# Kernel tuning notes

Hardware: AMD Instinct MI355X
Metric: run time of the kernel (lower is better)

The kernel has to match this reference:

```python
import jax, jax.numpy as jnp
import numpy as np

B, L, H, E, K = 64, 200, 256, 8, 2
LN_EPS = 1e-5

def setup_inputs() -> dict:
    key = jax.random.key(0)
    ks = jax.random.split(key, 24)
    r = lambda k, *s: jax.random.normal(k, s, dtype=jnp.float32)
    w = lambda k, *s: 0.02 * jax.random.normal(k, s, dtype=jnp.float32)
    return {
        'text_emb': r(ks[0], B, L, H),
        'img_emb': r(ks[1], B, L, H),
        'item_emb': r(ks[2], B, L, H),
        'noise_t': r(ks[3], B, L, H),
        'noise_i': r(ks[4], B, L, H),
        'W_mu_t': w(ks[5], H, H), 'b_mu_t': jnp.zeros((H,), jnp.float32),
        'W_sg_t': w(ks[6], H, H), 'b_sg_t': jnp.zeros((H,), jnp.float32),
        'W_mu_i': w(ks[7], H, H), 'b_mu_i': jnp.zeros((H,), jnp.float32),
        'W_sg_i': w(ks[8], H, H), 'b_sg_i': jnp.zeros((H,), jnp.float32),
        'W_gate': w(ks[9], H, E), 'b_gate': jnp.zeros((E,), jnp.float32),
        'W_texp': w(ks[10], E, H, H), 'b_texp': jnp.zeros((E, H), jnp.float32),
        'W_iexp': w(ks[11], E, H, H), 'b_iexp': jnp.zeros((E, H), jnp.float32),
        'W_fuse': w(ks[12], 2 * H, H), 'b_fuse': jnp.zeros((H,), jnp.float32),
        'ln_g': jnp.ones((H,), jnp.float32), 'ln_b': jnp.zeros((H,), jnp.float32),
    }

def _topk_routing(z, W_gate, b_gate):
    # softmax over experts, keep top-k, renormalize (matches torch scatter_ version)
    weights = jax.nn.softmax(z @ W_gate + b_gate, axis=-1)   # [B,L,E]
    top_w, idx = jax.lax.top_k(weights, K)                   # [B,L,K]
    sparse = jnp.sum(jax.nn.one_hot(idx, E, dtype=weights.dtype) * top_w[..., None], axis=-2)
    return sparse / (jnp.sum(sparse, axis=-1, keepdims=True) + 1e-8)

def _layernorm(x, g, b):
    mu = jnp.mean(x, axis=-1, keepdims=True)
    var = jnp.mean(jnp.square(x - mu), axis=-1, keepdims=True)
    return (x - mu) * jax.lax.rsqrt(var + LN_EPS) * g + b

def reference(text_emb, img_emb, item_emb, noise_t, noise_i,
              W_mu_t, b_mu_t, W_sg_t, b_sg_t, W_mu_i, b_mu_i, W_sg_i, b_sg_i,
              W_gate, b_gate, W_texp, b_texp, W_iexp, b_iexp,
              W_fuse, b_fuse, ln_g, ln_b):
    # VAE-style reparameterization per modality
    t_mu = text_emb @ W_mu_t + b_mu_t
    t_sigma = jnp.exp(text_emb @ W_sg_t + b_sg_t)
    i_mu = img_emb @ W_mu_i + b_mu_i
    i_sigma = jnp.exp(img_emb @ W_sg_i + b_sg_i)
    t_z = t_mu + t_sigma * noise_t
    i_z = i_mu + i_sigma * noise_i
    # top-k gating
    t_gate = _topk_routing(t_z, W_gate, b_gate)   # [B,L,E]
    i_gate = _topk_routing(i_z, W_gate, b_gate)
    # dense all-expert stack + gated combine
    t_experts = jnp.einsum('blh,ehd->bled', t_z, W_texp) + b_texp  # [B,L,E,H]
    t_out = jnp.einsum('bled,ble->bld', t_experts, t_gate)
    i_experts = jnp.einsum('blh,ehd->bled', i_z, W_iexp) + b_iexp
    i_out = jnp.einsum('bled,ble->bld', i_experts, i_gate)
    # fusion: Linear(2H->H) -> LayerNorm -> ReLU, residual with item_emb
    cat = jnp.concatenate([t_out, i_out], axis=-1)
    fused = jax.nn.relu(_layernorm(cat @ W_fuse + b_fuse, ln_g, ln_b))
    fusion = item_emb + fused
    return fusion, t_mu, t_sigma, i_mu, i_sigma
```

## Files before the change

### kernel.cpp

```cpp
#include <hip/hip_runtime.h>
#include <hip/hip_bf16.h>
#include <math.h>

#define NTOK 12800
#define HD 256
#define SOUT (NTOK * HD)

typedef __attribute__((ext_vector_type(8))) short short8_t;
typedef __attribute__((ext_vector_type(4))) float f32x4;

__device__ __forceinline__ unsigned short f2b(float f) {
    union { float f; unsigned u; } v; v.f = f;
    unsigned r = (v.u + 0x7FFFu + ((v.u >> 16) & 1u)) >> 16;
    return (unsigned short)r;
}
__device__ __forceinline__ float b2f(unsigned short s) {
    union { unsigned u; float f; } v; v.u = ((unsigned)s) << 16;
    return v.f;
}
__device__ __forceinline__ void glds16(const void* g, void* l) {
    __builtin_amdgcn_global_load_lds(
        (const __attribute__((address_space(1))) void*)g,
        (__attribute__((address_space(3))) void*)l, 16, 0, 0);
}

__global__ __launch_bounds__(256) void prepW_kernel(
    const float* __restrict__ W_texp, const float* __restrict__ W_iexp,
    const float* __restrict__ W_mu_t, const float* __restrict__ W_sg_t,
    const float* __restrict__ W_mu_i, const float* __restrict__ W_sg_i,
    const float* __restrict__ W_fuse,
    unsigned short* __restrict__ wt_t, unsigned short* __restrict__ wt_i,
    unsigned short* __restrict__ wt_f,
    unsigned short* __restrict__ wpk_th, unsigned short* __restrict__ wpk_tl,
    unsigned short* __restrict__ wpk_ih, unsigned short* __restrict__ wpk_il)
{
    const int z = blockIdx.y;
    const float* src;
    unsigned short* dsth;
    unsigned short* dstl = nullptr;
    int dstride = 256, koff = 0, rowoff = 0;
    if (z < 8)       { src = W_texp + (size_t)z * 65536;       dsth = wt_t + (size_t)z * 65536; }
    else if (z < 16) { src = W_iexp + (size_t)(z - 8) * 65536; dsth = wt_i + (size_t)(z - 8) * 65536; }
    else if (z == 16){ src = W_mu_t; dsth = wpk_th; dstl = wpk_tl; }
    else if (z == 17){ src = W_sg_t; dsth = wpk_th; dstl = wpk_tl; rowoff = 256; }
    else if (z == 18){ src = W_mu_i; dsth = wpk_ih; dstl = wpk_il; }
    else if (z == 19){ src = W_sg_i; dsth = wpk_ih; dstl = wpk_il; rowoff = 256; }
    else if (z == 20){ src = W_fuse;         dsth = wt_f; dstride = 512; koff = 0;   }
    else             { src = W_fuse + 65536; dsth = wt_f; dstride = 512; koff = 256; }

    const int tk = (blockIdx.x >> 2) * 64;
    const int td = (blockIdx.x & 3) * 64;
    __shared__ float T[64][68];
    const int t = threadIdx.x;
    {
        const int r = t >> 2, c0 = (t & 3) * 16;
        const float* s = &src[(size_t)(tk + r) * 256 + td + c0];
#pragma unroll
        for (int j = 0; j < 4; ++j)
            *reinterpret_cast<float4*>(&T[r][c0 + j * 4]) =
                *reinterpret_cast<const float4*>(&s[j * 4]);
    }
    __syncthreads();
    {
        const int d = t & 63, kc = (t >> 6) * 16;
        union { unsigned short s[16]; short8_t v[2]; } uh, ul;
#pragma unroll
        for (int j = 0; j < 16; ++j) {
            const float x = T[kc + j][d];
            uh.s[j] = f2b(x);
            ul.s[j] = f2b(x - b2f(uh.s[j]));
        }
        unsigned short* p = &dsth[(size_t)(rowoff + td + d) * dstride + koff + tk + kc];
        *reinterpret_cast<short8_t*>(p) = uh.v[0];
        *reinterpret_cast<short8_t*>(p + 8) = uh.v[1];
        if (dstl) {
            unsigned short* q = &dstl[(size_t)(rowoff + td + d) * 256 + tk + kc];
            *reinterpret_cast<short8_t*>(q) = ul.v[0];
            *reinterpret_cast<short8_t*>(q + 8) = ul.v[1];
        }
    }
}

__global__ __launch_bounds__(256) void cvt_kernel(
    const float* __restrict__ text, const float* __restrict__ img,
    unsigned short* __restrict__ ah_t, unsigned short* __restrict__ al_t,
    unsigned short* __restrict__ ah_i, unsigned short* __restrict__ al_i)
{
    const int mod = blockIdx.y;
    const float* src = mod ? img : text;
    unsigned short* dh = mod ? ah_i : ah_t;
    unsigned short* dl = mod ? al_i : al_t;
    const size_t base = ((size_t)blockIdx.x * 256 + threadIdx.x) * 8;
    const float4 v0 = *reinterpret_cast<const float4*>(&src[base]);
    const float4 v1 = *reinterpret_cast<const float4*>(&src[base + 4]);
    const float x[8] = { v0.x, v0.y, v0.z, v0.w, v1.x, v1.y, v1.z, v1.w };
    union { unsigned short u[8]; short8_t v; } qh, ql;
#pragma unroll
    for (int c = 0; c < 8; ++c) {
        qh.u[c] = f2b(x[c]);
        ql.u[c] = f2b(x[c] - b2f(qh.u[c]));
    }
    *reinterpret_cast<short8_t*>(&dh[base]) = qh.v;
    *reinterpret_cast<short8_t*>(&dl[base]) = ql.v;
}

__global__ __launch_bounds__(256) void reparam_mfma_kernel(
    const unsigned short* __restrict__ ah_t, const unsigned short* __restrict__ al_t,
    const unsigned short* __restrict__ ah_i, const unsigned short* __restrict__ al_i,
    const unsigned short* __restrict__ wpk_th, const unsigned short* __restrict__ wpk_tl,
    const unsigned short* __restrict__ wpk_ih, const unsigned short* __restrict__ wpk_il,
    const float* __restrict__ b_mu_t, const float* __restrict__ b_sg_t,
    const float* __restrict__ b_mu_i, const float* __restrict__ b_sg_i,
    float* __restrict__ o_tmu, float* __restrict__ o_tsig,
    float* __restrict__ o_imu, float* __restrict__ o_isig)
{
    const int mod = blockIdx.z;
    const unsigned short* Ah = mod ? ah_i : ah_t;
    const unsigned short* Al = mod ? al_i : al_t;
    const unsigned short* Wh = mod ? wpk_ih : wpk_th;
    const unsigned short* Wl = mod ? wpk_il : wpk_tl;
    const float* bmu = mod ? b_mu_i : b_mu_t;
    const float* bsg = mod ? b_sg_i : b_sg_t;
    float* omu = mod ? o_imu : o_tmu;
    float* osg = mod ? o_isig : o_tsig;

    __shared__ __align__(16) unsigned short AhS[2][4][64][8];
    __shared__ __align__(16) unsigned short AlS[2][4][64][8];
    __shared__ __align__(16) unsigned short BhS[2][4][128][8];
    __shared__ __align__(16) unsigned short BlS[2][4][128][8];

    const int tid = threadIdx.x;
    const int lane = tid & 63;
    const int w = tid >> 6;
    const int wr = w >> 1, wc = w & 1;
    const int lg = lane >> 4;
    const int lr = lane & 15;
    const int m0 = blockIdx.x * 64;
    const int n0 = blockIdx.y * 128;

    const int ar = tid >> 2, akc = tid & 3;
    const int bn = tid >> 1, bk0 = (tid & 1) * 2;

    {
        *reinterpret_cast<short8_t*>(&AhS[0][akc][ar][0]) =
            *reinterpret_cast<const short8_t*>(&Ah[(size_t)(m0 + ar) * HD + akc * 8]);
        *reinterpret_cast<short8_t*>(&AlS[0][akc][ar][0]) =
            *reinterpret_cast<const short8_t*>(&Al[(size_t)(m0 + ar) * HD + akc * 8]);
#pragma unroll
        for (int j = 0; j < 2; ++j) {
            const int kc = bk0 + j;
            *reinterpret_cast<short8_t*>(&BhS[0][kc][bn][0]) =
                *reinterpret_cast<const short8_t*>(&Wh[(size_t)(n0 + bn) * HD + kc * 8]);
            *reinterpret_cast<short8_t*>(&BlS[0][kc][bn][0]) =
                *reinterpret_cast<const short8_t*>(&Wl[(size_t)(n0 + bn) * HD + kc * 8]);
        }
    }
    __syncthreads();

    f32x4 acc[2][4];
#pragma unroll
    for (int mi = 0; mi < 2; ++mi)
#pragma unroll
        for (int ni = 0; ni < 4; ++ni)
            acc[mi][ni] = (f32x4){0.f, 0.f, 0.f, 0.f};

    for (int ks = 0; ks < 8; ++ks) {
        const int cur = ks & 1;
        short8_t rah, ral, rbh[2], rbl[2];
        if (ks < 7) {
            const int k1 = (ks + 1) * 32;
            rah = *reinterpret_cast<const short8_t*>(&Ah[(size_t)(m0 + ar) * HD + k1 + akc * 8]);
            ral = *reinterpret_cast<const short8_t*>(&Al[(size_t)(m0 + ar) * HD + k1 + akc * 8]);
#pragma unroll
            for (int j = 0; j < 2; ++j) {
                const int kc = bk0 + j;
                rbh[j] = *reinterpret_cast<const short8_t*>(&Wh[(size_t)(n0 + bn) * HD + k1 + kc * 8]);
                rbl[j] = *reinterpret_cast<const short8_t*>(&Wl[(size_t)(n0 + bn) * HD + k1 + kc * 8]);
            }
        }
        short8_t ahf[2], alf[2], bhf[4], blf[4];
#pragma unroll
        for (int mi = 0; mi < 2; ++mi) {
            ahf[mi] = *reinterpret_cast<const short8_t*>(&AhS[cur][lg][wr * 32 + mi * 16 + lr][0]);
            alf[mi] = *reinterpret_cast<const short8_t*>(&AlS[cur][lg][wr * 32 + mi * 16 + lr][0]);
        }
#pragma unroll
        for (int ni = 0; ni < 4; ++ni) {
            bhf[ni] = *reinterpret_cast<const short8_t*>(&BhS[cur][lg][wc * 64 + ni * 16 + lr][0]);
            blf[ni] = *reinterpret_cast<const short8_t*>(&BlS[cur][lg][wc * 64 + ni * 16 + lr][0]);
        }
#pragma unroll
        for (int mi = 0; mi < 2; ++mi)
#pragma unroll
            for (int ni = 0; ni < 4; ++ni) {
                acc[mi][ni] = __builtin_amdgcn_mfma_f32_16x16x32_bf16(ahf[mi], bhf[ni], acc[mi][ni], 0, 0, 0);
                acc[mi][ni] = __builtin_amdgcn_mfma_f32_16x16x32_bf16(ahf[mi], blf[ni], acc[mi][ni], 0, 0, 0);
                acc[mi][ni] = __builtin_amdgcn_mfma_f32_16x16x32_bf16(alf[mi], bhf[ni], acc[mi][ni], 0, 0, 0);
            }
        if (ks < 7) {
            const int nxt = cur ^ 1;
            *reinterpret_cast<short8_t*>(&AhS[nxt][akc][ar][0]) = rah;
            *reinterpret_cast<short8_t*>(&AlS[nxt][akc][ar][0]) = ral;
#pragma unroll
            for (int j = 0; j < 2; ++j) {
                const int kc = bk0 + j;
                *reinterpret_cast<short8_t*>(&BhS[nxt][kc][bn][0]) = rbh[j];
                *reinterpret_cast<short8_t*>(&BlS[nxt][kc][bn][0]) = rbl[j];
            }
        }
        __syncthreads();
    }

    const bool is_sg = (n0 >= 256);
    float bv[4];
    int cc[4];
#pragma unroll
    for (int ni = 0; ni < 4; ++ni) {
        const int dpk = n0 + wc * 64 + ni * 16 + lr;
        cc[ni] = is_sg ? dpk - 256 : dpk;
        bv[ni] = is_sg ? bsg[cc[ni]] : bmu[cc[ni]];
    }
    float* outp = is_sg ? osg : omu;
#pragma unroll
    for (int mi = 0; mi < 2; ++mi)
#pragma unroll
        for (int r = 0; r < 4; ++r) {
            const int row = m0 + wr * 32 + mi * 16 + lg * 4 + r;
#pragma unroll
            for (int ni = 0; ni < 4; ++ni) {
                const float v = acc[mi][ni][r] + bv[ni];
                outp[(size_t)row * HD + cc[ni]] = is_sg ? expf(v) : v;
            }
        }
}

__global__ __launch_bounds__(256) void gate_kernel(
    const float* __restrict__ o_tmu, const float* __restrict__ o_tsig,
    const float* __restrict__ o_imu, const float* __restrict__ o_isig,
    const float* __restrict__ noise_t, const float* __restrict__ noise_i,
    const float* __restrict__ Wg, const float* __restrict__ bg,
    float* __restrict__ t_gate, float* __restrict__ i_gate,
    unsigned short* __restrict__ tzb, unsigned short* __restrict__ izb)
{
    const int mod = blockIdx.y;
    const float* mu    = mod ? o_imu  : o_tmu;
    const float* sig   = mod ? o_isig : o_tsig;
    const float* noise = mod ? noise_i : noise_t;
    float* gate        = mod ? i_gate : t_gate;
    unsigned short* zb = mod ? izb : tzb;

    const int lane = threadIdx.x & 63;
    const int n = blockIdx.x * 4 + (threadIdx.x >> 6);
    const size_t off = (size_t)n * HD + lane * 4;
    const float4 m4 = *reinterpret_cast<const float4*>(&mu[off]);
    const float4 s4 = *reinterpret_cast<const float4*>(&sig[off]);
    const float4 n4 = *reinterpret_cast<const float4*>(&noise[off]);
    const float zz[4] = { fmaf(s4.x, n4.x, m4.x), fmaf(s4.y, n4.y, m4.y),
                          fmaf(s4.z, n4.z, m4.z), fmaf(s4.w, n4.w, m4.w) };
    ushort4 zb4;
    zb4.x = f2b(zz[0]); zb4.y = f2b(zz[1]); zb4.z = f2b(zz[2]); zb4.w = f2b(zz[3]);
    *reinterpret_cast<ushort4*>(&zb[off]) = zb4;

    float lg[8];
#pragma unroll
    for (int e = 0; e < 8; ++e) lg[e] = 0.f;
#pragma unroll
    for (int i = 0; i < 4; ++i) {
        const float* wr = &Wg[(size_t)(lane * 4 + i) * 8];
        const float4 w0 = *reinterpret_cast<const float4*>(wr);
        const float4 w1 = *reinterpret_cast<const float4*>(wr + 4);
        lg[0] = fmaf(zz[i], w0.x, lg[0]); lg[1] = fmaf(zz[i], w0.y, lg[1]);
        lg[2] = fmaf(zz[i], w0.z, lg[2]); lg[3] = fmaf(zz[i], w0.w, lg[3]);
        lg[4] = fmaf(zz[i], w1.x, lg[4]); lg[5] = fmaf(zz[i], w1.y, lg[5]);
        lg[6] = fmaf(zz[i], w1.z, lg[6]); lg[7] = fmaf(zz[i], w1.w, lg[7]);
    }
#pragma unroll
    for (int off2 = 32; off2; off2 >>= 1)
#pragma unroll
        for (int e = 0; e < 8; ++e) lg[e] += __shfl_down(lg[e], off2);

    if (lane == 0) {
        float m = -1e30f;
#pragma unroll
        for (int e = 0; e < 8; ++e) { lg[e] += bg[e]; m = fmaxf(m, lg[e]); }
        float p[8], s = 0.f;
#pragma unroll
        for (int e = 0; e < 8; ++e) { p[e] = expf(lg[e] - m); s += p[e]; }
        const float inv_s = 1.f / s;
#pragma unroll
        for (int e = 0; e < 8; ++e) p[e] *= inv_s;
        int e1 = 0;
#pragma unroll
        for (int e = 1; e < 8; ++e) if (p[e] > p[e1]) e1 = e;
        int e2 = (e1 == 0) ? 1 : 0;
#pragma unroll
        for (int e = 0; e < 8; ++e) if (e != e1 && p[e] > p[e2]) e2 = e;
        const float denom = 1.f / (p[e1] + p[e2] + 1e-8f);
        float g[8];
#pragma unroll
        for (int e = 0; e < 8; ++e) g[e] = 0.f;
        g[e1] = p[e1] * denom; g[e2] = p[e2] * denom;
        float* gr = &gate[(size_t)n * 8];
        *reinterpret_cast<float4*>(gr)     = make_float4(g[0], g[1], g[2], g[3]);
        *reinterpret_cast<float4*>(gr + 4) = make_float4(g[4], g[5], g[6], g[7]);
    }
}

__global__ __launch_bounds__(256) void expert_mfma_kernel(
    const unsigned short* __restrict__ tzb, const unsigned short* __restrict__ izb,
    const unsigned short* __restrict__ wt_t, const unsigned short* __restrict__ wt_i,
    const float* __restrict__ bx_t, const float* __restrict__ bx_i,
    const float* __restrict__ g_t, const float* __restrict__ g_i,
    unsigned short* __restrict__ out_t, unsigned short* __restrict__ out_i)
{
    const int mod = blockIdx.z;
    const unsigned short* Zb = mod ? izb : tzb;
    const unsigned short* Wt = mod ? wt_i : wt_t;
    const float* bx   = mod ? bx_i : bx_t;
    const float* gate = mod ? g_i  : g_t;
    unsigned short* outp = mod ? out_i : out_t;

    __shared__ __align__(16) unsigned short Ab[2][512][8];
    __shared__ __align__(16) unsigned short Bb[2][512][8];
    __shared__ float gld[128][8];

    const int tid = threadIdx.x;
    const int lane = tid & 63;
    const int w = tid >> 6;
    const int wr = w >> 1, wc = w & 1;
    const int lg = lane >> 4;
    const int lr = lane & 15;
    const int m0 = blockIdx.x * 128;
    const int n0 = blockIdx.y * 128;

    reinterpret_cast<float4*>(&gld[0][0])[tid] =
        reinterpret_cast<const float4*>(&gate[(size_t)m0 * 8])[tid];

    const int c0 = w * 64 + lane;
    const int row0 = c0 >> 2,          kc0 = c0 & 3;
    const int row1 = (c0 + 256) >> 2,  kc1 = (c0 + 256) & 3;

#define STAGE(buf, e_, ks_)                                                    \
    {                                                                          \
        const unsigned short* We_ = Wt + (size_t)(e_) * 65536 + (size_t)n0 * HD;\
        glds16(&Zb[(size_t)(m0 + row0) * HD + (ks_) * 32 + kc0 * 8],           \
               &Ab[buf][w * 64][0]);                                           \
        glds16(&Zb[(size_t)(m0 + row1) * HD + (ks_) * 32 + kc1 * 8],           \
               &Ab[buf][256 + w * 64][0]);                                     \
        glds16(&We_[(size_t)row0 * HD + (ks_) * 32 + kc0 * 8],                 \
               &Bb[buf][w * 64][0]);                                           \
        glds16(&We_[(size_t)row1 * HD + (ks_) * 32 + kc1 * 8],                 \
               &Bb[buf][256 + w * 64][0]);                                     \
    }

    STAGE(0, 0, 0);
    __syncthreads();

    f32x4 acc[4][4], accT[4][4];
#pragma unroll
    for (int mi = 0; mi < 4; ++mi)
#pragma unroll
        for (int ni = 0; ni < 4; ++ni) {
            acc[mi][ni]  = (f32x4){0.f, 0.f, 0.f, 0.f};
            accT[mi][ni] = (f32x4){0.f, 0.f, 0.f, 0.f};
        }

    for (int kk = 0; kk < 64; ++kk) {
        const int cur = kk & 1;
        const int e = kk >> 3, ks = kk & 7;
        if (kk < 63) {
            const int e2 = (kk + 1) >> 3, ks2 = (kk + 1) & 7;
            STAGE(cur ^ 1, e2, ks2);
        }
        short8_t af[4], bf[4];
#pragma unroll
        for (int mi = 0; mi < 4; ++mi)
            af[mi] = *reinterpret_cast<const short8_t*>(
                &Ab[cur][(wr * 64 + mi * 16 + lr) * 4 + lg][0]);
#pragma unroll
        for (int ni = 0; ni < 4; ++ni)
            bf[ni] = *reinterpret_cast<const short8_t*>(
                &Bb[cur][(wc * 64 + ni * 16 + lr) * 4 + lg][0]);
#pragma unroll
        for (int mi = 0; mi < 4; ++mi)
#pragma unroll
            for (int ni = 0; ni < 4; ++ni)
                acc[mi][ni] = __builtin_amdgcn_mfma_f32_16x16x32_bf16(
                    af[mi], bf[ni], acc[mi][ni], 0, 0, 0);
        if (ks == 7) {
#pragma unroll
            for (int mi = 0; mi < 4; ++mi) {
                const int rb = wr * 64 + mi * 16 + lg * 4;
                const float gv0 = gld[rb + 0][e];
                const float gv1 = gld[rb + 1][e];
                const float gv2 = gld[rb + 2][e];
                const float gv3 = gld[rb + 3][e];
#pragma unroll
                for (int ni = 0; ni < 4; ++ni) {
                    const float bv = bx[(size_t)e * HD + n0 + wc * 64 + ni * 16 + lr];
                    accT[mi][ni][0] += gv0 * (acc[mi][ni][0] + bv);
                    accT[mi][ni][1] += gv1 * (acc[mi][ni][1] + bv);
                    accT[mi][ni][2] += gv2 * (acc[mi][ni][2] + bv);
                    accT[mi][ni][3] += gv3 * (acc[mi][ni][3] + bv);
                    acc[mi][ni] = (f32x4){0.f, 0.f, 0.f, 0.f};
                }
            }
        }
        __syncthreads();
    }
#undef STAGE

#pragma unroll
    for (int mi = 0; mi < 4; ++mi)
#pragma unroll
        for (int ni = 0; ni < 4; ++ni)
#pragma unroll
            for (int r = 0; r < 4; ++r)
                outp[(size_t)(m0 + wr * 64 + mi * 16 + lg * 4 + r) * HD
                     + n0 + wc * 64 + ni * 16 + lr] = f2b(accT[mi][ni][r]);
}

__global__ __launch_bounds__(256) void fusegemm_mfma_kernel(
    const unsigned short* __restrict__ t_outb, const unsigned short* __restrict__ i_outb,
    const unsigned short* __restrict__ wtf, const float* __restrict__ bfuse,
    float* __restrict__ fused)
{
    __shared__ __align__(16) unsigned short AS[2][8][64][8];
    __shared__ __align__(16) unsigned short BS[2][8][128][8];

    const int tid = threadIdx.x;
    const int lane = tid & 63;
    const int w = tid >> 6;
    const int wr = w >> 1, wc = w & 1;
    const int lg = lane >> 4;
    const int lr = lane & 15;
    const int m0 = blockIdx.x * 64;
    const int n0 = blockIdx.y * 128;

    const int ar = tid >> 2, akc0 = (tid & 3) * 2;
    const int bn = tid >> 1, bkc0 = (tid & 1) * 4;

    {
        const unsigned short* base = t_outb;
#pragma unroll
        for (int j = 0; j < 2; ++j) {
            const int kc = akc0 + j;
            *reinterpret_cast<short8_t*>(&AS[0][kc][ar][0]) =
                *reinterpret_cast<const short8_t*>(&base[(size_t)(m0 + ar) * HD + kc * 8]);
        }
#pragma unroll
        for (int j = 0; j < 4; ++j) {
            const int kc = bkc0 + j;
            *reinterpret_cast<short8_t*>(&BS[0][kc][bn][0]) =
                *reinterpret_cast<const short8_t*>(&wtf[(size_t)(n0 + bn) * 512 + kc * 8]);
        }
    }
    __syncthreads();

    f32x4 acc[2][4];
#pragma unroll
    for (int mi = 0; mi < 2; ++mi)
#pragma unroll
        for (int ni = 0; ni < 4; ++ni)
            acc[mi][ni] = (f32x4){0.f, 0.f, 0.f, 0.f};

    for (int ks = 0; ks < 8; ++ks) {
        const int cur = ks & 1;
        short8_t ra[2], rbv[4];
        if (ks < 7) {
            const int ks2 = ks + 1;
            const unsigned short* base = (ks2 < 4) ? t_outb : i_outb;
            const int kloc = (ks2 & 3) * 64;
#pragma unroll
            for (int j = 0; j < 2; ++j) {
                const int kc = akc0 + j;
                ra[j] = *reinterpret_cast<const short8_t*>(
                    &base[(size_t)(m0 + ar) * HD + kloc + kc * 8]);
            }
#pragma unroll
            for (int j = 0; j < 4; ++j) {
                const int kc = bkc0 + j;
                rbv[j] = *reinterpret_cast<const short8_t*>(
                    &wtf[(size_t)(n0 + bn) * 512 + ks2 * 64 + kc * 8]);
            }
        }
#pragma unroll
        for (int s = 0; s < 2; ++s) {
            short8_t af[2], bf[4];
#pragma unroll
            for (int mi = 0; mi < 2; ++mi)
                af[mi] = *reinterpret_cast<const short8_t*>(
                    &AS[cur][s * 4 + lg][wr * 32 + mi * 16 + lr][0]);
#pragma unroll
            for (int ni = 0; ni < 4; ++ni)
                bf[ni] = *reinterpret_cast<const short8_t*>(
                    &BS[cur][s * 4 + lg][wc * 64 + ni * 16 + lr][0]);
#pragma unroll
            for (int mi = 0; mi < 2; ++mi)
#pragma unroll
                for (int ni = 0; ni < 4; ++ni)
                    acc[mi][ni] = __builtin_amdgcn_mfma_f32_16x16x32_bf16(
                        af[mi], bf[ni], acc[mi][ni], 0, 0, 0);
        }
        if (ks < 7) {
            const int nxt = cur ^ 1;
#pragma unroll
            for (int j = 0; j < 2; ++j)
                *reinterpret_cast<short8_t*>(&AS[nxt][akc0 + j][ar][0]) = ra[j];
#pragma unroll
            for (int j = 0; j < 4; ++j)
                *reinterpret_cast<short8_t*>(&BS[nxt][bkc0 + j][bn][0]) = rbv[j];
        }
        __syncthreads();
    }

    float bv[4];
    int cc[4];
#pragma unroll
    for (int ni = 0; ni < 4; ++ni) {
        cc[ni] = n0 + wc * 64 + ni * 16 + lr;
        bv[ni] = bfuse[cc[ni]];
    }
#pragma unroll
    for (int mi = 0; mi < 2; ++mi)
#pragma unroll
        for (int r = 0; r < 4; ++r) {
            const int row = m0 + wr * 32 + mi * 16 + lg * 4 + r;
#pragma unroll
            for (int ni = 0; ni < 4; ++ni)
                fused[(size_t)row * HD + cc[ni]] = acc[mi][ni][r] + bv[ni];
        }
}

__global__ __launch_bounds__(256) void ln_relu_res_kernel(
    const float* __restrict__ fused, const float* __restrict__ g,
    const float* __restrict__ b, const float* __restrict__ item,
    float* __restrict__ fusion)
{
    const int lane = threadIdx.x & 63;
    const int n = blockIdx.x * 4 + (threadIdx.x >> 6);
    const size_t off = (size_t)n * HD + lane * 4;
    const float4 x = *reinterpret_cast<const float4*>(&fused[off]);
    float s = x.x + x.y + x.z + x.w;
    float ss = x.x * x.x + x.y * x.y + x.z * x.z + x.w * x.w;
#pragma unroll
    for (int o = 32; o; o >>= 1) { s += __shfl_xor(s, o); ss += __shfl_xor(ss, o); }
    const float mean = s * (1.f / 256.f);
    const float var = ss * (1.f / 256.f) - mean * mean;
    const float rstd = rsqrtf(var + 1e-5f);
    const float4 gg = *reinterpret_cast<const float4*>(&g[lane * 4]);
    const float4 bb = *reinterpret_cast<const float4*>(&b[lane * 4]);
    const float4 it = *reinterpret_cast<const float4*>(&item[off]);
    float4 o4;
    o4.x = fmaxf((x.x - mean) * rstd * gg.x + bb.x, 0.f) + it.x;
    o4.y = fmaxf((x.y - mean) * rstd * gg.y + bb.y, 0.f) + it.y;
    o4.z = fmaxf((x.z - mean) * rstd * gg.z + bb.z, 0.f) + it.z;
    o4.w = fmaxf((x.w - mean) * rstd * gg.w + bb.w, 0.f) + it.w;
    *reinterpret_cast<float4*>(&fusion[off]) = o4;
}

extern "C" void kernel_launch(void* const* d_in, const int* in_sizes, int n_in,
                              void* d_out, int out_size, void* d_ws, size_t ws_size,
                              hipStream_t stream)
{
    const float* text    = (const float*)d_in[0];
    const float* img     = (const float*)d_in[1];
    const float* item    = (const float*)d_in[2];
    const float* noise_t = (const float*)d_in[3];
    const float* noise_i = (const float*)d_in[4];
    const float* W_mu_t  = (const float*)d_in[5];
    const float* b_mu_t  = (const float*)d_in[6];
    const float* W_sg_t  = (const float*)d_in[7];
    const float* b_sg_t  = (const float*)d_in[8];
    const float* W_mu_i  = (const float*)d_in[9];
    const float* b_mu_i  = (const float*)d_in[10];
    const float* W_sg_i  = (const float*)d_in[11];
    const float* b_sg_i  = (const float*)d_in[12];
    const float* W_gate  = (const float*)d_in[13];
    const float* b_gate  = (const float*)d_in[14];
    const float* W_texp  = (const float*)d_in[15];
    const float* b_texp  = (const float*)d_in[16];
    const float* W_iexp  = (const float*)d_in[17];
    const float* b_iexp  = (const float*)d_in[18];
    const float* W_fuse  = (const float*)d_in[19];
    const float* b_fuse  = (const float*)d_in[20];
    const float* ln_g    = (const float*)d_in[21];
    const float* ln_b    = (const float*)d_in[22];

    float* out    = (float*)d_out;
    float* fusion = out;
    float* o_tmu  = out + (size_t)SOUT;
    float* o_tsig = out + (size_t)2 * SOUT;
    float* o_imu  = out + (size_t)3 * SOUT;
    float* o_isig = out + (size_t)4 * SOUT;

    unsigned short* bufA = (unsigned short*)d_ws;
    unsigned short* bufB = bufA + (size_t)SOUT;
    unsigned short* bufC = bufB + (size_t)SOUT;
    unsigned short* tzb  = bufC + (size_t)2 * SOUT;
    unsigned short* izb  = tzb + (size_t)SOUT;
    float* t_gate = (float*)(izb + (size_t)SOUT);
    float* i_gate = t_gate + (size_t)NTOK * 8;
    unsigned short* wt_t   = (unsigned short*)(i_gate + (size_t)NTOK * 8);
    unsigned short* wt_i   = wt_t + (size_t)8 * 65536;
    unsigned short* wt_f   = wt_i + (size_t)8 * 65536;
    unsigned short* wpk_th = wt_f + (size_t)131072;
    unsigned short* wpk_tl = wpk_th + (size_t)131072;
    unsigned short* wpk_ih = wpk_tl + (size_t)131072;
    unsigned short* wpk_il = wpk_ih + (size_t)131072;

    unsigned short* ah_t = bufA;
    unsigned short* al_t = bufB;
    unsigned short* ah_i = bufC;
    unsigned short* al_i = bufC + (size_t)SOUT;
    unsigned short* t_outb = bufA;
    unsigned short* i_outb = bufB;
    float* fused = (float*)bufC;

    prepW_kernel<<<dim3(16, 22), 256, 0, stream>>>(
        W_texp, W_iexp, W_mu_t, W_sg_t, W_mu_i, W_sg_i, W_fuse,
        wt_t, wt_i, wt_f, wpk_th, wpk_tl, wpk_ih, wpk_il);

    cvt_kernel<<<dim3(SOUT / 2048, 2), 256, 0, stream>>>(
        text, img, ah_t, al_t, ah_i, al_i);

    reparam_mfma_kernel<<<dim3(NTOK / 64, 4, 2), 256, 0, stream>>>(
        ah_t, al_t, ah_i, al_i, wpk_th, wpk_tl, wpk_ih, wpk_il,
        b_mu_t, b_sg_t, b_mu_i, b_sg_i,
        o_tmu, o_tsig, o_imu, o_isig);

    gate_kernel<<<dim3(NTOK / 4, 2), 256, 0, stream>>>(
        o_tmu, o_tsig, o_imu, o_isig, noise_t, noise_i,
        W_gate, b_gate, t_gate, i_gate, tzb, izb);

    expert_mfma_kernel<<<dim3(NTOK / 128, 2, 2), 256, 0, stream>>>(
        tzb, izb, wt_t, wt_i, b_texp, b_iexp, t_gate, i_gate, t_outb, i_outb);

    fusegemm_mfma_kernel<<<dim3(NTOK / 64, 2), 256, 0, stream>>>(
        t_outb, i_outb, wt_f, b_fuse, fused);

    ln_relu_res_kernel<<<NTOK / 4, 256, 0, stream>>>(fused, ln_g, ln_b, item, fusion);
}
```

Before: 152.7 us.

## Replace dense all-expert GEMM with sparse top-2 routed expert GEMM

The gate kernel now uses atomics to build per-expert token lists with their weights, instead of writing a dense gate matrix. A new expert kernel gathers only the routed tokens for each expert and runs one 256-K GEMM per expert chunk. Each token's two expert outputs go into separate slots, and the fusion GEMM adds them in bf16 while loading. This removes the 4x redundant expert FLOPs of the dense stack. In exchange it adds gathered loads, atomics, an extra zero kernel, and a bf16 rounding of each partial before the sum, which changes numerics slightly.

```diff
diff --git a/kernel.cpp b/kernel.cpp
--- a/kernel.cpp
+++ b/kernel.cpp
@@ -22,6 +22,17 @@
     __builtin_amdgcn_global_load_lds(
         (const __attribute__((address_space(1))) void*)g,
         (__attribute__((address_space(3))) void*)l, 16, 0, 0);
+}
+__device__ __forceinline__ short8_t add_bf16x8(short8_t a, short8_t b) {
+    union { unsigned short u[8]; short8_t v; } ua, ub, r;
+    ua.v = a; ub.v = b;
+#pragma unroll
+    for (int i = 0; i < 8; ++i) r.u[i] = f2b(b2f(ua.u[i]) + b2f(ub.u[i]));
+    return r.v;
+}
+
+__global__ void zero_cnt_kernel(unsigned* __restrict__ cnt) {
+    cnt[threadIdx.x] = 0;
 }
 
 __global__ __launch_bounds__(256) void prepW_kernel(
@@ -239,14 +250,14 @@
     const float* __restrict__ o_imu, const float* __restrict__ o_isig,
     const float* __restrict__ noise_t, const float* __restrict__ noise_i,
     const float* __restrict__ Wg, const float* __restrict__ bg,
-    float* __restrict__ t_gate, float* __restrict__ i_gate,
-    unsigned short* __restrict__ tzb, unsigned short* __restrict__ izb)
+    unsigned short* __restrict__ tzb, unsigned short* __restrict__ izb,
+    unsigned* __restrict__ idx_list, float* __restrict__ wgt_list,
+    unsigned* __restrict__ cnt)
 {
     const int mod = blockIdx.y;
     const float* mu    = mod ? o_imu  : o_tmu;
     const float* sig   = mod ? o_isig : o_tsig;
     const float* noise = mod ? noise_i : noise_t;
-    float* gate        = mod ? i_gate : t_gate;
     unsigned short* zb = mod ? izb : tzb;
 
     const int lane = threadIdx.x & 63;
@@ -296,33 +307,44 @@
 #pragma unroll
         for (int e = 0; e < 8; ++e) if (e != e1 && p[e] > p[e2]) e2 = e;
         const float denom = 1.f / (p[e1] + p[e2] + 1e-8f);
-        float g[8];
-#pragma unroll
-        for (int e = 0; e < 8; ++e) g[e] = 0.f;
-        g[e1] = p[e1] * denom; g[e2] = p[e2] * denom;
-        float* gr = &gate[(size_t)n * 8];
-        *reinterpret_cast<float4*>(gr)     = make_float4(g[0], g[1], g[2], g[3]);
-        *reinterpret_cast<float4*>(gr + 4) = make_float4(g[4], g[5], g[6], g[7]);
-    }
-}
-
-__global__ __launch_bounds__(256) void expert_mfma_kernel(
+        const int s1 = mod * 8 + e1;
+        const int s2 = mod * 8 + e2;
+        const unsigned p1 = atomicAdd(&cnt[s1 * 32], 1u);
+        idx_list[(size_t)s1 * NTOK + p1] = (unsigned)(n * 2 + 0);
+        wgt_list[(size_t)s1 * NTOK + p1] = p[e1] * denom;
+        const unsigned p2 = atomicAdd(&cnt[s2 * 32], 1u);
+        idx_list[(size_t)s2 * NTOK + p2] = (unsigned)(n * 2 + 1);
+        wgt_list[(size_t)s2 * NTOK + p2] = p[e2] * denom;
+    }
+}
+
+__global__ __launch_bounds__(256) void expert_sparse_kernel(
     const unsigned short* __restrict__ tzb, const unsigned short* __restrict__ izb,
     const unsigned short* __restrict__ wt_t, const unsigned short* __restrict__ wt_i,
     const float* __restrict__ bx_t, const float* __restrict__ bx_i,
-    const float* __restrict__ g_t, const float* __restrict__ g_i,
-    unsigned short* __restrict__ out_t, unsigned short* __restrict__ out_i)
-{
+    const unsigned* __restrict__ idx_list, const float* __restrict__ wgt_list,
+    const unsigned* __restrict__ cnt,
+    unsigned short* __restrict__ slot_t, unsigned short* __restrict__ slot_i)
+{
+    const int chunk = blockIdx.x;
+    const int e  = blockIdx.y >> 1;
+    const int nh = blockIdx.y & 1;
     const int mod = blockIdx.z;
+    const int seg = mod * 8 + e;
+    const unsigned cnt_e = cnt[seg * 32];
+    if ((unsigned)(chunk * 128) >= cnt_e) return;
+
     const unsigned short* Zb = mod ? izb : tzb;
     const unsigned short* Wt = mod ? wt_i : wt_t;
-    const float* bx   = mod ? bx_i : bx_t;
-    const float* gate = mod ? g_i  : g_t;
-    unsigned short* outp = mod ? out_i : out_t;
+    const float* bx = mod ? bx_i : bx_t;
+    unsigned short* outp = mod ? slot_i : slot_t;
+    const int n0 = nh * 128;
+    const size_t sb = (size_t)seg * NTOK + (size_t)chunk * 128;
 
     __shared__ __align__(16) unsigned short Ab[2][512][8];
     __shared__ __align__(16) unsigned short Bb[2][512][8];
-    __shared__ float gld[128][8];
+    __shared__ float gw[128];
+    __shared__ unsigned il[128];
 
     const int tid = threadIdx.x;
     const int lane = tid & 63;
@@ -330,48 +352,47 @@
     const int wr = w >> 1, wc = w & 1;
     const int lg = lane >> 4;
     const int lr = lane & 15;
-    const int m0 = blockIdx.x * 128;
-    const int n0 = blockIdx.y * 128;
-
-    reinterpret_cast<float4*>(&gld[0][0])[tid] =
-        reinterpret_cast<const float4*>(&gate[(size_t)m0 * 8])[tid];
+
+    if (tid < 128) {
+        const bool v = (unsigned)(chunk * 128 + tid) < cnt_e;
+        il[tid] = v ? idx_list[sb + tid] : (unsigned)(2 * NTOK);
+        gw[tid] = v ? wgt_list[sb + tid] : 0.f;
+    }
 
     const int c0 = w * 64 + lane;
-    const int row0 = c0 >> 2,          kc0 = c0 & 3;
-    const int row1 = (c0 + 256) >> 2,  kc1 = (c0 + 256) & 3;
-
-#define STAGE(buf, e_, ks_)                                                    \
+    const int row0 = c0 >> 2,         kc0 = c0 & 3;
+    const int row1 = (c0 + 256) >> 2, kc1 = (c0 + 256) & 3;
+    const unsigned i0 = ((unsigned)(chunk * 128 + row0) < cnt_e)
+                        ? idx_list[sb + row0] : (unsigned)(2 * NTOK);
+    const unsigned i1 = ((unsigned)(chunk * 128 + row1) < cnt_e)
+                        ? idx_list[sb + row1] : (unsigned)(2 * NTOK);
+    const size_t atok0 = (size_t)(i0 >> 1) * HD;
+    const size_t atok1 = (size_t)(i1 >> 1) * HD;
+    const unsigned short* We_ = Wt + (size_t)e * 65536 + (size_t)n0 * HD;
+
+#define SSTAGE(buf, ks_)                                                       \
     {                                                                          \
-        const unsigned short* We_ = Wt + (size_t)(e_) * 65536 + (size_t)n0 * HD;\
-        glds16(&Zb[(size_t)(m0 + row0) * HD + (ks_) * 32 + kc0 * 8],           \
-               &Ab[buf][w * 64][0]);                                           \
-        glds16(&Zb[(size_t)(m0 + row1) * HD + (ks_) * 32 + kc1 * 8],           \
-               &Ab[buf][256 + w * 64][0]);                                     \
+        glds16(&Zb[atok0 + (ks_) * 32 + kc0 * 8], &Ab[buf][w * 64][0]);        \
+        glds16(&Zb[atok1 + (ks_) * 32 + kc1 * 8], &Ab[buf][256 + w * 64][0]);  \
         glds16(&We_[(size_t)row0 * HD + (ks_) * 32 + kc0 * 8],                 \
                &Bb[buf][w * 64][0]);                                           \
         glds16(&We_[(size_t)row1 * HD + (ks_) * 32 + kc1 * 8],                 \
                &Bb[buf][256 + w * 64][0]);                                     \
     }
 
-    STAGE(0, 0, 0);
+    SSTAGE(0, 0);
     __syncthreads();
 
-    f32x4 acc[4][4], accT[4][4];
+    f32x4 acc[4][4];
 #pragma unroll
     for (int mi = 0; mi < 4; ++mi)
 #pragma unroll
-        for (int ni = 0; ni < 4; ++ni) {
-            acc[mi][ni]  = (f32x4){0.f, 0.f, 0.f, 0.f};
-            accT[mi][ni] = (f32x4){0.f, 0.f, 0.f, 0.f};
-        }
-
-    for (int kk = 0; kk < 64; ++kk) {
-        const int cur = kk & 1;
-        const int e = kk >> 3, ks = kk & 7;
-        if (kk < 63) {
-            const int e2 = (kk + 1) >> 3, ks2 = (kk + 1) & 7;
-            STAGE(cur ^ 1, e2, ks2);
-        }
+        for (int ni = 0; ni < 4; ++ni)
+            acc[mi][ni] = (f32x4){0.f, 0.f, 0.f, 0.f};
+
+    for (int ks = 0; ks < 8; ++ks) {
+        const int cur = ks & 1;
+        if (ks < 7) SSTAGE(cur ^ 1, ks + 1);
         short8_t af[4], bf[4];
 #pragma unroll
         for (int mi = 0; mi < 4; ++mi)
@@ -387,41 +408,30 @@
             for (int ni = 0; ni < 4; ++ni)
                 acc[mi][ni] = __builtin_amdgcn_mfma_f32_16x16x32_bf16(
                     af[mi], bf[ni], acc[mi][ni], 0, 0, 0);
-        if (ks == 7) {
-#pragma unroll
-            for (int mi = 0; mi < 4; ++mi) {
-                const int rb = wr * 64 + mi * 16 + lg * 4;
-                const float gv0 = gld[rb + 0][e];
-                const float gv1 = gld[rb + 1][e];
-                const float gv2 = gld[rb + 2][e];
-                const float gv3 = gld[rb + 3][e];
-#pragma unroll
-                for (int ni = 0; ni < 4; ++ni) {
-                    const float bv = bx[(size_t)e * HD + n0 + wc * 64 + ni * 16 + lr];
-                    accT[mi][ni][0] += gv0 * (acc[mi][ni][0] + bv);
-                    accT[mi][ni][1] += gv1 * (acc[mi][ni][1] + bv);
-                    accT[mi][ni][2] += gv2 * (acc[mi][ni][2] + bv);
-                    accT[mi][ni][3] += gv3 * (acc[mi][ni][3] + bv);
-                    acc[mi][ni] = (f32x4){0.f, 0.f, 0.f, 0.f};
-                }
-            }
-        }
         __syncthreads();
     }
-#undef STAGE
-
+#undef SSTAGE
+
+    float bv[4];
+#pragma unroll
+    for (int ni = 0; ni < 4; ++ni)
+        bv[ni] = bx[(size_t)e * HD + n0 + wc * 64 + ni * 16 + lr];
 #pragma unroll
     for (int mi = 0; mi < 4; ++mi)
 #pragma unroll
-        for (int ni = 0; ni < 4; ++ni)
-#pragma unroll
-            for (int r = 0; r < 4; ++r)
-                outp[(size_t)(m0 + wr * 64 + mi * 16 + lg * 4 + r) * HD
-                     + n0 + wc * 64 + ni * 16 + lr] = f2b(accT[mi][ni][r]);
+        for (int r = 0; r < 4; ++r) {
+            const int row_local = wr * 64 + mi * 16 + lg * 4 + r;
+            const float wv = gw[row_local];
+            const size_t tb = (size_t)il[row_local] * HD;
+#pragma unroll
+            for (int ni = 0; ni < 4; ++ni)
+                outp[tb + n0 + wc * 64 + ni * 16 + lr] =
+                    f2b(wv * (acc[mi][ni][r] + bv[ni]));
+        }
 }
 
 __global__ __launch_bounds__(256) void fusegemm_mfma_kernel(
-    const unsigned short* __restrict__ t_outb, const unsigned short* __restrict__ i_outb,
+    const unsigned short* __restrict__ slot_t, const unsigned short* __restrict__ slot_i,
     const unsigned short* __restrict__ wtf, const float* __restrict__ bfuse,
     float* __restrict__ fused)
 {
@@ -439,14 +449,15 @@
 
     const int ar = tid >> 2, akc0 = (tid & 3) * 2;
     const int bn = tid >> 1, bkc0 = (tid & 1) * 4;
+    const size_t tb = (size_t)(m0 + ar) * 2 * HD;
 
     {
-        const unsigned short* base = t_outb;
 #pragma unroll
         for (int j = 0; j < 2; ++j) {
             const int kc = akc0 + j;
-            *reinterpret_cast<short8_t*>(&AS[0][kc][ar][0]) =
-                *reinterpret_cast<const short8_t*>(&base[(size_t)(m0 + ar) * HD + kc * 8]);
+            const short8_t s0 = *reinterpret_cast<const short8_t*>(&slot_t[tb + kc * 8]);
+            const short8_t s1 = *reinterpret_cast<const short8_t*>(&slot_t[tb + HD + kc * 8]);
+            *reinterpret_cast<short8_t*>(&AS[0][kc][ar][0]) = add_bf16x8(s0, s1);
         }
 #pragma unroll
         for (int j = 0; j < 4; ++j) {
@@ -469,13 +480,16 @@
         short8_t ra[2], rbv[4];
         if (ks < 7) {
             const int ks2 = ks + 1;
-            const unsigned short* base = (ks2 < 4) ? t_outb : i_outb;
+            const unsigned short* sp = (ks2 < 4) ? slot_t : slot_i;
             const int kloc = (ks2 & 3) * 64;
 #pragma unroll
             for (int j = 0; j < 2; ++j) {
                 const int kc = akc0 + j;
-                ra[j] = *reinterpret_cast<const short8_t*>(
-                    &base[(size_t)(m0 + ar) * HD + kloc + kc * 8]);
+                const short8_t s0 = *reinterpret_cast<const short8_t*>(
+                    &sp[tb + kloc + kc * 8]);
+                const short8_t s1 = *reinterpret_cast<const short8_t*>(
+                    &sp[tb + HD + kloc + kc * 8]);
+                ra[j] = add_bf16x8(s0, s1);
             }
 #pragma unroll
             for (int j = 0; j < 4; ++j) {
@@ -594,28 +608,29 @@
     float* o_imu  = out + (size_t)3 * SOUT;
     float* o_isig = out + (size_t)4 * SOUT;
 
-    unsigned short* bufA = (unsigned short*)d_ws;
-    unsigned short* bufB = bufA + (size_t)SOUT;
-    unsigned short* bufC = bufB + (size_t)SOUT;
-    unsigned short* tzb  = bufC + (size_t)2 * SOUT;
-    unsigned short* izb  = tzb + (size_t)SOUT;
-    float* t_gate = (float*)(izb + (size_t)SOUT);
-    float* i_gate = t_gate + (size_t)NTOK * 8;
-    unsigned short* wt_t   = (unsigned short*)(i_gate + (size_t)NTOK * 8);
+    const size_t SLOTPAD = (size_t)(2 * NTOK + 256) * HD;
+    unsigned short* slot_t = (unsigned short*)d_ws;
+    unsigned short* slot_i = slot_t + SLOTPAD;
+    unsigned short* tzb    = slot_i + SLOTPAD;
+    unsigned short* izb    = tzb + (size_t)SOUT;
+    unsigned short* wt_t   = izb + (size_t)SOUT;
     unsigned short* wt_i   = wt_t + (size_t)8 * 65536;
     unsigned short* wt_f   = wt_i + (size_t)8 * 65536;
     unsigned short* wpk_th = wt_f + (size_t)131072;
     unsigned short* wpk_tl = wpk_th + (size_t)131072;
     unsigned short* wpk_ih = wpk_tl + (size_t)131072;
     unsigned short* wpk_il = wpk_ih + (size_t)131072;
-
-    unsigned short* ah_t = bufA;
-    unsigned short* al_t = bufB;
-    unsigned short* ah_i = bufC;
-    unsigned short* al_i = bufC + (size_t)SOUT;
-    unsigned short* t_outb = bufA;
-    unsigned short* i_outb = bufB;
-    float* fused = (float*)bufC;
+    unsigned* idx_list = (unsigned*)(wpk_il + (size_t)131072);
+    float*    wgt_list = (float*)(idx_list + (size_t)16 * NTOK);
+    unsigned* cnt      = (unsigned*)(wgt_list + (size_t)16 * NTOK);
+
+    unsigned short* ah_t = slot_t;
+    unsigned short* al_t = slot_t + (size_t)SOUT;
+    unsigned short* ah_i = slot_i;
+    unsigned short* al_i = slot_i + (size_t)SOUT;
+    float* fused = (float*)tzb;
+
+    zero_cnt_kernel<<<1, 512, 0, stream>>>(cnt);
 
     prepW_kernel<<<dim3(16, 22), 256, 0, stream>>>(
         W_texp, W_iexp, W_mu_t, W_sg_t, W_mu_i, W_sg_i, W_fuse,
@@ -631,13 +646,14 @@
 
     gate_kernel<<<dim3(NTOK / 4, 2), 256, 0, stream>>>(
         o_tmu, o_tsig, o_imu, o_isig, noise_t, noise_i,
-        W_gate, b_gate, t_gate, i_gate, tzb, izb);
-
-    expert_mfma_kernel<<<dim3(NTOK / 128, 2, 2), 256, 0, stream>>>(
-        tzb, izb, wt_t, wt_i, b_texp, b_iexp, t_gate, i_gate, t_outb, i_outb);
+        W_gate, b_gate, tzb, izb, idx_list, wgt_list, cnt);
+
+    expert_sparse_kernel<<<dim3(100, 16, 2), 256, 0, stream>>>(
+        tzb, izb, wt_t, wt_i, b_texp, b_iexp,
+        idx_list, wgt_list, cnt, slot_t, slot_i);
 
     fusegemm_mfma_kernel<<<dim3(NTOK / 64, 2), 256, 0, stream>>>(
-        t_outb, i_outb, wt_f, b_fuse, fused);
+        slot_t, slot_i, wt_f, b_fuse, fused);
 
     ln_relu_res_kernel<<<NTOK / 4, 256, 0, stream>>>(fused, ln_g, ln_b, item, fusion);
 }
```

New measurement: 180.4 us. 18.1% more time.
